# Kernel optimization log

Measured on AMD Instinct MI355X. Metric: run time of the kernel, lower is better.

The kernel has to match this reference:

```python
import jax, jax.numpy as jnp
import numpy as np

B, S, D, H = 4, 4096, 1024, 64

def setup_inputs() -> dict:
    key = jax.random.key(0)
    k1, k2, k3, k4 = jax.random.split(key, 4)
    inp = {
        'input': jax.random.normal(k1, (B, S, D), dtype=jnp.float32),
        'Wq': jax.random.normal(k2, (D, H), dtype=jnp.float32) * (D ** -0.5),
        'Wk': jax.random.normal(k3, (D, H), dtype=jnp.float32) * (D ** -0.5),
        'Wv': jax.random.normal(k4, (D, H), dtype=jnp.float32) * (D ** -0.5),
    }
    return inp

def reference(input, Wq, Wk, Wv):
    # Projections: [B,S,D] @ [D,H] -> [B,S,H]
    q = input @ Wq
    k = input @ Wk
    v = input @ Wv
    head_size = Wq.shape[-1]
    # Scaled scores: [B,S,S]
    scores = jnp.einsum('bqh,bkh->bqk', q, k) * (head_size ** -0.5)
    seq_len = input.shape[1]
    causal = jnp.tril(jnp.ones((seq_len, seq_len), dtype=bool))
    masked = jnp.where(causal, scores, -jnp.inf)
    weights = jax.nn.softmax(masked, axis=-1)
    # dropout p=0.0 -> identity
    return jnp.einsum('bqk,bkh->bqh', weights, v)
```

## Files before the change

kernel.cpp:

```cpp
#include <hip/hip_runtime.h>

#define NS 8

typedef __attribute__((ext_vector_type(8))) short sh8;
typedef __attribute__((ext_vector_type(4))) short sh4;
typedef __attribute__((ext_vector_type(4))) float f4;

#define QSCALE 0.18033688011112042f

typedef const __attribute__((address_space(1))) unsigned int* gas_t;
typedef __attribute__((address_space(3))) unsigned int* las_t;
#define GLD16(g, l) __builtin_amdgcn_global_load_lds((gas_t)(g), (las_t)(l), 16, 0, 0)

static __device__ __forceinline__ unsigned short f2bf(float f) {
  unsigned u = __builtin_bit_cast(unsigned, f);
  u += 0x7fffu + ((u >> 16) & 1u);
  return (unsigned short)(u >> 16);
}
static __device__ __forceinline__ float bf2f(unsigned short s) {
  unsigned u = ((unsigned)s) << 16;
  return __builtin_bit_cast(float, u);
}

__global__ __launch_bounds__(256) void wt_kernel(const float* __restrict__ Wq,
                                                 const float* __restrict__ Wk,
                                                 const float* __restrict__ Wv,
                                                 unsigned short* __restrict__ Wt2) {
  int blk = blockIdx.x;
  int band = blk >> 3;
  int widx = band >> 2;
  const float* W = widx == 0 ? Wq : (widx == 1 ? Wk : Wv);
  int ncol = (band & 3) * 16;
  int t = threadIdx.x;
  int kt = (blk & 7) * 4 + (t >> 6);
  int lane = t & 63, q = lane >> 4, l15 = lane & 15;
  const float* src = W + (size_t)(kt * 32 + q * 8) * 64 + ncol + l15;
  sh8 o;
#pragma unroll
  for (int j = 0; j < 8; ++j) o[j] = (short)f2bf(src[(size_t)j * 64]);
  *(sh8*)&Wt2[((size_t)(band * 32 + kt) * 64 + lane) * 8] = o;
}

__global__ __launch_bounds__(256, 4) void proj_kernel(const float* __restrict__ in,
                                                      const unsigned short* __restrict__ Wt2,
                                                      unsigned short* __restrict__ Qg,
                                                      unsigned short* __restrict__ Kg,
                                                      unsigned short* __restrict__ Vtg) {
  __shared__ __align__(16) char lds[28672];
  int t = threadIdx.x;
  int w = t >> 6, lane = t & 63, q = lane >> 4, l15 = lane & 15;
  int m0 = blockIdx.x * 16;

  const float* ga = in + (size_t)(m0 + l15) * 1024 + q * 8 + (w & 1) * 4;
  const unsigned short* gb = Wt2 + (size_t)(w * 3) * 16384 + lane * 8;

  f4 acc[3];
  f4 z = {0.f, 0.f, 0.f, 0.f};
#pragma unroll
  for (int nt = 0; nt < 3; ++nt) acc[nt] = z;

#define STAGE(kt, buf)                                                        \
  {                                                                           \
    int k0 = (kt) * 32;                                                       \
    char* base = lds + (buf) * 14336;                                         \
    if (w < 2) GLD16(ga + k0, base + w * 1024);                               \
    GLD16(gb + (kt) * 512, base + 2048 + (w * 3 + 0) * 1024);                 \
    GLD16(gb + 16384 + (kt) * 512, base + 2048 + (w * 3 + 1) * 1024);         \
    GLD16(gb + 32768 + (kt) * 512, base + 2048 + (w * 3 + 2) * 1024);         \
  }

  STAGE(0, 0);
  for (int kt = 0; kt < 32; ++kt) {
    int cur = kt & 1;
    __syncthreads();
    if (kt + 1 < 32) STAGE(kt + 1, cur ^ 1);

    const f4* Af = (const f4*)(lds + cur * 14336);
    f4 lo = Af[lane], hi = Af[64 + lane];
    sh8 a;
#pragma unroll
    for (int j = 0; j < 4; ++j) {
      a[j] = (short)f2bf(lo[j]);
      a[4 + j] = (short)f2bf(hi[j]);
    }
    const sh8* Bf = (const sh8*)(lds + cur * 14336 + 2048);
#pragma unroll
    for (int nt = 0; nt < 3; ++nt) {
      sh8 bf = Bf[(w * 3 + nt) * 64 + lane];
      acc[nt] = __builtin_amdgcn_mfma_f32_16x16x32_bf16(a, bf, acc[nt], 0, 0, 0);
    }
  }
#undef STAGE

  float* vred = (float*)lds;
#pragma unroll
  for (int nt = 0; nt < 3; ++nt) {
    int band = w * 3 + nt;
#pragma unroll
    for (int r = 0; r < 4; ++r) {
      int row = q * 4 + r;
      float v = acc[nt][r];
      if (band < 4) {
        Qg[(size_t)(m0 + row) * 64 + band * 16 + l15] = f2bf(v * QSCALE);
      } else if (band < 8) {
        Kg[(size_t)(m0 + row) * 64 + (band - 4) * 16 + l15] = f2bf(v);
      } else {
        vred[row * 69 + (band - 8) * 16 + l15] = v;
      }
    }
  }
  __syncthreads();
  {
    int h = t >> 2, sl = (t & 3) * 4;
    int bb = m0 >> 12, s0 = m0 & 4095;
    sh4 vv;
#pragma unroll
    for (int j = 0; j < 4; ++j) vv[j] = (short)f2bf(vred[(sl + j) * 69 + h]);
    *(sh4*)&Vtg[(((size_t)(bb * 64 + h)) << 12) + s0 + sl] = vv;
  }
}

__global__ __launch_bounds__(256, 4) void attn_split(const unsigned short* __restrict__ Qg,
                                                     const unsigned short* __restrict__ Kg,
                                                     const unsigned short* __restrict__ Vtg,
                                                     unsigned short* __restrict__ Opart,
                                                     float* __restrict__ Lpart) {
  __shared__ unsigned short Ks[64 * 72];
  __shared__ unsigned short Vs[64 * 72];
  __shared__ unsigned short Pw[4 * 16 * 72];
  int t = threadIdx.x;
  int b = blockIdx.y;
  int qt = 63 - (int)(blockIdx.x >> 3);
  int sp = blockIdx.x & 7;
  int wave = t >> 6, lane = t & 63, quad = lane >> 4, l15 = lane & 15;
  unsigned short* Pws = Pw + wave * 16 * 72;

  int qrow0 = qt * 64 + wave * 16;
  size_t pbase = ((size_t)sp * 4 + b) * 4096;

  int nkt = qt + 1;
  int chunk = (nkt + NS - 1) / NS;
  int t0 = sp * chunk, t1 = min(nkt, t0 + chunk);
  if (t0 >= t1) {
#pragma unroll
    for (int r = 0; r < 4; ++r) {
      size_t row = pbase + qrow0 + quad * 4 + r;
#pragma unroll
      for (int ht = 0; ht < 4; ++ht) Opart[row * 64 + ht * 16 + l15] = 0;
      if (l15 == 0) Lpart[row] = 0.f;
    }
    return;
  }

  sh8 qa[2];
#pragma unroll
  for (int ks = 0; ks < 2; ++ks)
    qa[ks] = *(const sh8*)&Qg[(size_t)((b << 12) + qrow0 + l15) * 64 + ks * 32 + quad * 8];

  sh8 ones;
#pragma unroll
  for (int j = 0; j < 8; ++j) ones[j] = (short)0x3F80;

  f4 o[5];
  f4 z = {0.f, 0.f, 0.f, 0.f};
#pragma unroll
  for (int ht = 0; ht < 5; ++ht) o[ht] = z;

  int r0 = t >> 3, o0 = (t & 7) * 8;
  int r1 = (t + 256) >> 3, o1 = ((t + 256) & 7) * 8;
  const unsigned short* kg0 = Kg + (size_t)((b << 12) + r0) * 64 + o0;
  const unsigned short* kg1 = Kg + (size_t)((b << 12) + r1) * 64 + o1;
  const unsigned short* vg0 = Vtg + (((size_t)(b * 64 + r0)) << 12) + o0;
  const unsigned short* vg1 = Vtg + (((size_t)(b * 64 + r1)) << 12) + o1;

  sh8 kr0, kr1, vr0, vr1;
  {
    size_t ko = (size_t)t0 * 64 * 64;
    kr0 = *(const sh8*)(kg0 + ko); kr1 = *(const sh8*)(kg1 + ko);
    vr0 = *(const sh8*)(vg0 + t0 * 64); vr1 = *(const sh8*)(vg1 + t0 * 64);
  }

  for (int kt = t0; kt < t1; ++kt) {
    __syncthreads();
    *(sh8*)&Ks[r0 * 72 + o0] = kr0;
    *(sh8*)&Ks[r1 * 72 + o1] = kr1;
    *(sh8*)&Vs[r0 * 72 + o0] = vr0;
    *(sh8*)&Vs[r1 * 72 + o1] = vr1;
    if (kt + 1 < t1) {
      size_t ko = (size_t)(kt + 1) * 64 * 64;
      kr0 = *(const sh8*)(kg0 + ko); kr1 = *(const sh8*)(kg1 + ko);
      vr0 = *(const sh8*)(vg0 + (kt + 1) * 64); vr1 = *(const sh8*)(vg1 + (kt + 1) * 64);
    }
    __syncthreads();

    f4 st[4];
#pragma unroll
    for (int nt = 0; nt < 4; ++nt) st[nt] = z;
#pragma unroll
    for (int ks = 0; ks < 2; ++ks) {
#pragma unroll
      for (int nt = 0; nt < 4; ++nt) {
        sh8 kb = *(const sh8*)&Ks[(nt * 16 + l15) * 72 + ks * 32 + quad * 8];
        st[nt] = __builtin_amdgcn_mfma_f32_16x16x32_bf16(kb, qa[ks], st[nt], 0, 0, 0);
      }
    }

    if (kt == nkt - 1) {
      int qrow = qrow0 + l15;
#pragma unroll
      for (int nt = 0; nt < 4; ++nt) {
        int key0 = kt * 64 + nt * 16 + quad * 4;
#pragma unroll
        for (int r = 0; r < 4; ++r)
          if (key0 + r > qrow) st[nt][r] = -__builtin_inff();
      }
    }

#pragma unroll
    for (int nt = 0; nt < 4; ++nt) {
      sh4 pk;
#pragma unroll
      for (int r = 0; r < 4; ++r) pk[r] = (short)f2bf(exp2f(st[nt][r]));
      *(sh4*)&Pws[l15 * 72 + nt * 16 + quad * 4] = pk;
    }
    asm volatile("s_waitcnt lgkmcnt(0)" ::: "memory");

#pragma unroll
    for (int ks = 0; ks < 2; ++ks) {
      sh8 pa = *(const sh8*)&Pws[l15 * 72 + ks * 32 + quad * 8];
#pragma unroll
      for (int ht = 0; ht < 4; ++ht) {
        sh8 vb = *(const sh8*)&Vs[(ht * 16 + l15) * 72 + ks * 32 + quad * 8];
        o[ht] = __builtin_amdgcn_mfma_f32_16x16x32_bf16(pa, vb, o[ht], 0, 0, 0);
      }
      o[4] = __builtin_amdgcn_mfma_f32_16x16x32_bf16(pa, ones, o[4], 0, 0, 0);
    }
  }

#pragma unroll
  for (int r = 0; r < 4; ++r) {
    size_t row = pbase + qrow0 + quad * 4 + r;
#pragma unroll
    for (int ht = 0; ht < 4; ++ht)
      Opart[row * 64 + ht * 16 + l15] = f2bf(o[ht][r]);
    if (l15 == 0) Lpart[row] = o[4][r];
  }
}

__global__ __launch_bounds__(256) void attn_combine(const unsigned short* __restrict__ Opart,
                                                    const float* __restrict__ Lpart,
                                                    float* __restrict__ out) {
  int t = threadIdx.x;
  int rg = blockIdx.x * 4 + (t >> 6);
  int lane = t & 63;
  float acc = 0.f, L = 0.f;
#pragma unroll
  for (int s = 0; s < NS; ++s) {
    L += Lpart[(size_t)s * 16384 + rg];
    acc += bf2f(Opart[((size_t)s * 16384 + rg) * 64 + lane]);
  }
  out[(size_t)rg * 64 + lane] = acc / L;
}

extern "C" void kernel_launch(void* const* d_in, const int* in_sizes, int n_in,
                              void* d_out, int out_size, void* d_ws, size_t ws_size,
                              hipStream_t stream) {
  const float* in = (const float*)d_in[0];
  const float* Wq = (const float*)d_in[1];
  const float* Wk = (const float*)d_in[2];
  const float* Wv = (const float*)d_in[3];
  float* out = (float*)d_out;

  char* ws = (char*)d_ws;
  unsigned short* Wt2   = (unsigned short*)ws;
  unsigned short* Qg    = (unsigned short*)(ws + 393216);
  unsigned short* Kg    = (unsigned short*)(ws + 2490368);
  unsigned short* Vtg   = (unsigned short*)(ws + 4587520);
  unsigned short* Opart = (unsigned short*)(ws + 6684672);
  float*          Lpart = (float*)(ws + 23461888);

  hipLaunchKernelGGL(wt_kernel, dim3(96), dim3(256), 0, stream, Wq, Wk, Wv, Wt2);
  hipLaunchKernelGGL(proj_kernel, dim3(1024), dim3(256), 0, stream, in, Wt2, Qg, Kg, Vtg);
  hipLaunchKernelGGL(attn_split, dim3(64 * NS, 4), dim3(256), 0, stream,
                     Qg, Kg, Vtg, Opart, Lpart);
  hipLaunchKernelGGL(attn_combine, dim3(4096), dim3(256), 0, stream,
                     Opart, Lpart, out);
}
```

Before: 153.7 us.

## Compute 64 rows per block in projection kernel to reuse weight tiles

Each projection block now computes four 16-row M-tiles instead of one, holding the three weight fragments in registers and reusing them across all four tiles. The grid shrinks from 1024 to 256 blocks. This is meant to cut the repeated global/L2 reads of the full bf16 weight matrix, which every block previously streamed. The cost is more accumulator registers and LDS per block (occupancy hint lowered to 2) and only one block per CU, which may hurt latency hiding. The V-transpose store is widened to 8-element vectors.

```diff
diff --git a/kernel.cpp b/kernel.cpp
--- a/kernel.cpp
+++ b/kernel.cpp
@@ -41,32 +41,34 @@
   *(sh8*)&Wt2[((size_t)(band * 32 + kt) * 64 + lane) * 8] = o;
 }
 
-__global__ __launch_bounds__(256, 4) void proj_kernel(const float* __restrict__ in,
+__global__ __launch_bounds__(256, 2) void proj_kernel(const float* __restrict__ in,
                                                       const unsigned short* __restrict__ Wt2,
                                                       unsigned short* __restrict__ Qg,
                                                       unsigned short* __restrict__ Kg,
                                                       unsigned short* __restrict__ Vtg) {
-  __shared__ __align__(16) char lds[28672];
+  __shared__ __align__(16) char lds[40960];
   int t = threadIdx.x;
   int w = t >> 6, lane = t & 63, q = lane >> 4, l15 = lane & 15;
-  int m0 = blockIdx.x * 16;
-
-  const float* ga = in + (size_t)(m0 + l15) * 1024 + q * 8 + (w & 1) * 4;
+  int m0 = blockIdx.x * 64;
+
+  const float* ga0 = in + (size_t)(m0 + (w >> 1) * 16 + l15) * 1024 + q * 8 + (w & 1) * 4;
   const unsigned short* gb = Wt2 + (size_t)(w * 3) * 16384 + lane * 8;
 
-  f4 acc[3];
+  f4 acc[4][3];
   f4 z = {0.f, 0.f, 0.f, 0.f};
 #pragma unroll
-  for (int nt = 0; nt < 3; ++nt) acc[nt] = z;
+  for (int mt = 0; mt < 4; ++mt)
+#pragma unroll
+    for (int nt = 0; nt < 3; ++nt) acc[mt][nt] = z;
 
 #define STAGE(kt, buf)                                                        \
   {                                                                           \
-    int k0 = (kt) * 32;                                                       \
-    char* base = lds + (buf) * 14336;                                         \
-    if (w < 2) GLD16(ga + k0, base + w * 1024);                               \
-    GLD16(gb + (kt) * 512, base + 2048 + (w * 3 + 0) * 1024);                 \
-    GLD16(gb + 16384 + (kt) * 512, base + 2048 + (w * 3 + 1) * 1024);         \
-    GLD16(gb + 32768 + (kt) * 512, base + 2048 + (w * 3 + 2) * 1024);         \
+    char* base = lds + (buf) * 20480;                                         \
+    GLD16(ga0 + (kt) * 32, base + w * 1024);                                  \
+    GLD16(ga0 + 32768 + (kt) * 32, base + 4096 + w * 1024);                   \
+    GLD16(gb + (kt) * 512, base + 8192 + (w * 3 + 0) * 1024);                 \
+    GLD16(gb + 16384 + (kt) * 512, base + 8192 + (w * 3 + 1) * 1024);         \
+    GLD16(gb + 32768 + (kt) * 512, base + 8192 + (w * 3 + 2) * 1024);         \
   }
 
   STAGE(0, 0);
@@ -75,19 +77,24 @@
     __syncthreads();
     if (kt + 1 < 32) STAGE(kt + 1, cur ^ 1);
 
-    const f4* Af = (const f4*)(lds + cur * 14336);
-    f4 lo = Af[lane], hi = Af[64 + lane];
-    sh8 a;
-#pragma unroll
-    for (int j = 0; j < 4; ++j) {
-      a[j] = (short)f2bf(lo[j]);
-      a[4 + j] = (short)f2bf(hi[j]);
-    }
-    const sh8* Bf = (const sh8*)(lds + cur * 14336 + 2048);
-#pragma unroll
-    for (int nt = 0; nt < 3; ++nt) {
-      sh8 bf = Bf[(w * 3 + nt) * 64 + lane];
-      acc[nt] = __builtin_amdgcn_mfma_f32_16x16x32_bf16(a, bf, acc[nt], 0, 0, 0);
+    const f4* Af = (const f4*)(lds + cur * 20480);
+    const sh8* Bf = (const sh8*)(lds + cur * 20480 + 8192);
+    sh8 bfr[3];
+#pragma unroll
+    for (int nt = 0; nt < 3; ++nt) bfr[nt] = Bf[(w * 3 + nt) * 64 + lane];
+#pragma unroll
+    for (int mt = 0; mt < 4; ++mt) {
+      f4 lo = Af[mt * 128 + lane];
+      f4 hi = Af[mt * 128 + 64 + lane];
+      sh8 a;
+#pragma unroll
+      for (int j = 0; j < 4; ++j) {
+        a[j] = (short)f2bf(lo[j]);
+        a[4 + j] = (short)f2bf(hi[j]);
+      }
+#pragma unroll
+      for (int nt = 0; nt < 3; ++nt)
+        acc[mt][nt] = __builtin_amdgcn_mfma_f32_16x16x32_bf16(a, bfr[nt], acc[mt][nt], 0, 0, 0);
     }
   }
 #undef STAGE
@@ -97,26 +104,31 @@
   for (int nt = 0; nt < 3; ++nt) {
     int band = w * 3 + nt;
 #pragma unroll
-    for (int r = 0; r < 4; ++r) {
-      int row = q * 4 + r;
-      float v = acc[nt][r];
-      if (band < 4) {
-        Qg[(size_t)(m0 + row) * 64 + band * 16 + l15] = f2bf(v * QSCALE);
-      } else if (band < 8) {
-        Kg[(size_t)(m0 + row) * 64 + (band - 4) * 16 + l15] = f2bf(v);
-      } else {
-        vred[row * 69 + (band - 8) * 16 + l15] = v;
-      }
-    }
+    for (int mt = 0; mt < 4; ++mt)
+#pragma unroll
+      for (int r = 0; r < 4; ++r) {
+        int row = mt * 16 + q * 4 + r;
+        float v = acc[mt][nt][r];
+        if (band < 4) {
+          Qg[(size_t)(m0 + row) * 64 + band * 16 + l15] = f2bf(v * QSCALE);
+        } else if (band < 8) {
+          Kg[(size_t)(m0 + row) * 64 + (band - 4) * 16 + l15] = f2bf(v);
+        } else {
+          vred[row * 69 + (band - 8) * 16 + l15] = v;
+        }
+      }
   }
   __syncthreads();
   {
-    int h = t >> 2, sl = (t & 3) * 4;
+    int h = t >> 2, sl = (t & 3) * 16;
     int bb = m0 >> 12, s0 = m0 & 4095;
-    sh4 vv;
-#pragma unroll
-    for (int j = 0; j < 4; ++j) vv[j] = (short)f2bf(vred[(sl + j) * 69 + h]);
-    *(sh4*)&Vtg[(((size_t)(bb * 64 + h)) << 12) + s0 + sl] = vv;
+#pragma unroll
+    for (int half = 0; half < 2; ++half) {
+      sh8 vv;
+#pragma unroll
+      for (int j = 0; j < 8; ++j) vv[j] = (short)f2bf(vred[(sl + half * 8 + j) * 69 + h]);
+      *(sh8*)&Vtg[(((size_t)(bb * 64 + h)) << 12) + s0 + sl + half * 8] = vv;
+    }
   }
 }
 
@@ -280,7 +292,7 @@
   float*          Lpart = (float*)(ws + 23461888);
 
   hipLaunchKernelGGL(wt_kernel, dim3(96), dim3(256), 0, stream, Wq, Wk, Wv, Wt2);
-  hipLaunchKernelGGL(proj_kernel, dim3(1024), dim3(256), 0, stream, in, Wt2, Qg, Kg, Vtg);
+  hipLaunchKernelGGL(proj_kernel, dim3(256), dim3(256), 0, stream, in, Wt2, Qg, Kg, Vtg);
   hipLaunchKernelGGL(attn_split, dim3(64 * NS, 4), dim3(256), 0, stream,
                      Qg, Kg, Vtg, Opart, Lpart);
   hipLaunchKernelGGL(attn_combine, dim3(4096), dim3(256), 0, stream,
```

Result: slower. 157.2 us (+2.3%).
